# Performance work log

Measured on AMD Instinct MI355X. Metric: run time of the kernel, lower is better.

## Reference

```python
import jax, jax.numpy as jnp
import numpy as np

D_MODEL = 1024
NUM_HEADS = 16
D_K = D_MODEL // NUM_HEADS
THETA = 10000.0
B, T = 4, 2048


def apply_rope(x, positions):
    # x: [B, h, T, d_k], positions: [B, T] int
    half = D_K // 2
    inv_freq = 1.0 / (THETA ** (jnp.arange(half, dtype=jnp.float32) * 2.0 / D_K))  # [half]
    ang = positions.astype(jnp.float32)[:, None, :, None] * inv_freq  # [B,1,T,half]
    cos, sin = jnp.cos(ang), jnp.sin(ang)
    x1, x2 = x[..., 0::2], x[..., 1::2]  # even/odd interleaved pairs
    r1 = x1 * cos - x2 * sin
    r2 = x1 * sin + x2 * cos
    return jnp.stack([r1, r2], axis=-1).reshape(x.shape)


def setup_inputs() -> dict:
    key = jax.random.key(0)
    ks = jax.random.split(key, 5)
    scale = 1.0 / np.sqrt(D_MODEL)
    return {
        "in_features": jax.random.normal(ks[0], (B, T, D_MODEL), dtype=jnp.float32),
        "token_positions": jnp.broadcast_to(jnp.arange(T, dtype=jnp.int64), (B, T)),
        "Wq": jax.random.normal(ks[1], (D_MODEL, D_MODEL), dtype=jnp.float32) * scale,
        "Wk": jax.random.normal(ks[2], (D_MODEL, D_MODEL), dtype=jnp.float32) * scale,
        "Wv": jax.random.normal(ks[3], (D_MODEL, D_MODEL), dtype=jnp.float32) * scale,
        "Wo": jax.random.normal(ks[4], (D_MODEL, D_MODEL), dtype=jnp.float32) * scale,
    }


def reference(in_features, token_positions, Wq, Wk, Wv, Wo):
    x = in_features  # [B, T, d_model]
    # Linear stores weight [out, in]; y = x @ W.T (no bias)
    def proj(W):
        y = jnp.einsum('btd,ed->bte', x, W)
        return y.reshape(B, T, NUM_HEADS, D_K).transpose(0, 2, 1, 3)  # [B,h,T,d_k]
    Q, K, V = proj(Wq), proj(Wk), proj(Wv)
    Q = apply_rope(Q, token_positions)
    K = apply_rope(K, token_positions)
    scores = jnp.einsum('bhqd,bhkd->bhqk', Q, K) / jnp.sqrt(jnp.float32(D_K))
    causal = jnp.tril(jnp.ones((T, T), dtype=bool))  # True where allowed
    scores = jnp.where(causal, scores, jnp.float32(-1e30))
    attn = jax.nn.softmax(scores, axis=-1)
    heads = jnp.einsum('bhqk,bhkd->bhqd', attn, V)  # [B,h,T,d_k]
    out = heads.transpose(0, 2, 1, 3).reshape(B, T, D_MODEL)
    return jnp.einsum('btd,ed->bte', out, Wo)
```

## Files before the change

kernel.cpp:

```cpp
#include <hip/hip_runtime.h>
#include <cstdint>
#include <cstddef>

typedef unsigned short ushort_t;
typedef __attribute__((ext_vector_type(8))) short short8;
typedef __attribute__((ext_vector_type(4))) float f32x4;
typedef __attribute__((ext_vector_type(4))) _Float16 half4;
typedef __attribute__((ext_vector_type(8))) _Float16 half8;
typedef __attribute__((ext_vector_type(2))) _Float16 half2;
typedef __attribute__((ext_vector_type(2))) __fp16 fp16v2;
struct half4x2 { half4 lo, hi; };
struct half2x2 { half2 lo, hi; };

__device__ __forceinline__ unsigned short f2bf(float f) {
    unsigned u = __float_as_uint(f);
    u += 0x7fffu + ((u >> 16) & 1u);
    return (unsigned short)(u >> 16);
}
__device__ __forceinline__ float bf2f(unsigned short h) {
    return __uint_as_float((unsigned)h << 16);
}
__device__ __forceinline__ ushort_t f2h(float f) {
    _Float16 h = (_Float16)f;
    return __builtin_bit_cast(unsigned short, h);
}
__device__ __forceinline__ f32x4 zero4() {
    f32x4 z; z[0]=0.f; z[1]=0.f; z[2]=0.f; z[3]=0.f; return z;
}
__device__ __forceinline__ half4 pk4(float a, float b, float cc, float d) {
    half2x2 t;
    t.lo = __builtin_bit_cast(half2, (fp16v2)__builtin_amdgcn_cvt_pkrtz(a, b));
    t.hi = __builtin_bit_cast(half2, (fp16v2)__builtin_amdgcn_cvt_pkrtz(cc, d));
    return __builtin_bit_cast(half4, t);
}
__device__ __forceinline__ void gld_lds16(const ushort_t* g, ushort_t* l) {
    __builtin_amdgcn_global_load_lds(
        (const __attribute__((address_space(1))) void*)g,
        (__attribute__((address_space(3))) void*)l, 16, 0, 0);
}

__global__ void cvt_all(const float* __restrict__ x,
                        const float* __restrict__ wq, const float* __restrict__ wk,
                        const float* __restrict__ wv, const float* __restrict__ wo,
                        ushort_t* __restrict__ xb,
                        ushort_t* __restrict__ wqb, ushort_t* __restrict__ wkb,
                        ushort_t* __restrict__ wvb, ushort_t* __restrict__ wob,
                        float2* __restrict__ tab) {
    int idx = blockIdx.x * 256 + threadIdx.x;
    if (idx >= 3145728) {
        int i = idx - 3145728;
        int t = i >> 5, p = i & 31;
        float freq = __expf((float)p * -0.2878231366242557f);
        float sn, cs;
        sincosf((float)t * freq, &sn, &cs);
        tab[i] = make_float2(cs, sn);
        return;
    }
    const float* src; ushort_t* dst; int off;
    if (idx < 2097152) { src = x; dst = xb; off = idx; }
    else {
        int r = idx - 2097152;
        int w = r >> 18;
        off = r & 262143;
        src = (w == 0) ? wq : (w == 1) ? wk : (w == 2) ? wv : wo;
        dst = (w == 0) ? wqb : (w == 1) ? wkb : (w == 2) ? wvb : wob;
    }
    float4 v = ((const float4*)src)[off];
    ushort_t o[4];
    o[0] = f2bf(v.x); o[1] = f2bf(v.y); o[2] = f2bf(v.z); o[3] = f2bf(v.w);
    *(ushort4*)(dst + 4*(size_t)off) = *(const ushort4*)o;
}

__device__ __forceinline__ void gemm_core(const ushort_t* __restrict__ A,
                                          const ushort_t* __restrict__ W,
                                          ushort_t* As, ushort_t* Bs,
                                          int m0, int n0, f32x4 (&acc)[4][4]) {
    const int tid  = threadIdx.x;
    const int wave = tid >> 6, lane = tid & 63;
    const int wm = (wave >> 1) * 64, wn = (wave & 1) * 64;
    const int q = lane >> 4, c = lane & 15;
    const int srow = lane >> 3;
    const int gch  = (lane & 7) ^ srow;

    const ushort_t* ag = A + (size_t)(m0 + wave*8 + srow) * 1024 + gch*8;
    const ushort_t* bg = W + (size_t)(n0 + wave*8 + srow) * 1024 + gch*8;
    ushort_t* al = As + wave*512;
    ushort_t* bl = Bs + wave*512;

    for (int k0 = 0; k0 < 1024; k0 += 64) {
        __syncthreads();
#pragma unroll
        for (int n = 0; n < 4; ++n) gld_lds16(ag + (size_t)n*32768 + k0, al + n*2048);
#pragma unroll
        for (int n = 0; n < 4; ++n) gld_lds16(bg + (size_t)n*32768 + k0, bl + n*2048);
        asm volatile("s_waitcnt vmcnt(0)" ::: "memory");
        __syncthreads();

#pragma unroll
        for (int sk = 0; sk < 2; ++sk) {
            short8 af[4], bf[4];
#pragma unroll
            for (int i = 0; i < 4; ++i) {
                int row = wm + i*16 + c;
                af[i] = *(const short8*)(As + row*64 + (((sk*4 + q) ^ (row & 7)) * 8));
            }
#pragma unroll
            for (int j = 0; j < 4; ++j) {
                int row = wn + j*16 + c;
                bf[j] = *(const short8*)(Bs + row*64 + (((sk*4 + q) ^ (row & 7)) * 8));
            }
#pragma unroll
            for (int i = 0; i < 4; ++i)
#pragma unroll
                for (int j = 0; j < 4; ++j)
                    acc[i][j] = __builtin_amdgcn_mfma_f32_16x16x32_bf16(af[i], bf[j], acc[i][j], 0, 0, 0);
        }
    }
}

__device__ __forceinline__ void gemm_pipe256(const ushort_t* __restrict__ A,
                                             const ushort_t* __restrict__ W,
                                             ushort_t* __restrict__ As,
                                             ushort_t* __restrict__ Bs,
                                             int m0, int n0, f32x4 (&acc)[4][4]) {
    const int tid  = threadIdx.x;
    const int wave = tid >> 6, lane = tid & 63;
    const int wm = (wave >> 1) * 64, wn = (wave & 1) * 64;
    const int q = lane >> 4, c = lane & 15;
    const int srow = lane >> 3;
    const int gch  = (lane & 7) ^ srow;

    const ushort_t* ag = A + (size_t)(m0 + wave * 8 + srow) * 1024 + gch * 8;
    const ushort_t* bg = W + (size_t)(n0 + wave * 8 + srow) * 1024 + gch * 8;
    ushort_t* adst = As + wave * 512;
    ushort_t* bdst = Bs + wave * 512;

#pragma unroll
    for (int n = 0; n < 4; ++n) gld_lds16(ag + (size_t)n * 65536,      adst + n * 4096);
#pragma unroll
    for (int n = 0; n < 2; ++n) gld_lds16(bg + (size_t)n * 65536,      bdst + n * 4096);
#pragma unroll
    for (int n = 0; n < 4; ++n) gld_lds16(ag + (size_t)n * 65536 + 64, adst + 16384 + n * 4096);
#pragma unroll
    for (int n = 0; n < 2; ++n) gld_lds16(bg + (size_t)n * 65536 + 64, bdst + 8192 + n * 4096);
    asm volatile("s_waitcnt vmcnt(6)" ::: "memory");
    __builtin_amdgcn_s_barrier();

    const int ch0 = (q ^ (c & 7)) * 8;
    const int ch1 = ((4 + q) ^ (c & 7)) * 8;
    int cur = 0;
    for (int t = 0; t < 16; ++t) {
        const int nx2 = (cur >= 1) ? cur - 1 : 2;
        const ushort_t* ab = As + cur * 16384 + (wm + c) * 64;
        const ushort_t* bb = Bs + cur * 8192  + (wn + c) * 64;
        const int kc = (t + 2) * 64;
        const bool pf = (t < 14);
        short8 af[4], bf[4];

#pragma unroll
        for (int i = 0; i < 4; ++i) af[i] = *(const short8*)(ab + i * 1024 + ch0);
#pragma unroll
        for (int j = 0; j < 4; ++j) bf[j] = *(const short8*)(bb + j * 1024 + ch0);
        if (pf) {
            gld_lds16(ag + kc,           adst + nx2 * 16384);
            gld_lds16(ag + 65536 + kc,   adst + nx2 * 16384 + 4096);
            gld_lds16(bg + kc,           bdst + nx2 * 8192);
        }
        __builtin_amdgcn_s_barrier();
        asm volatile("s_waitcnt lgkmcnt(0)" ::: "memory");
        __builtin_amdgcn_s_setprio(1);
#pragma unroll
        for (int i = 0; i < 4; ++i)
#pragma unroll
            for (int j = 0; j < 4; ++j)
                acc[i][j] = __builtin_amdgcn_mfma_f32_16x16x32_bf16(af[i], bf[j], acc[i][j], 0, 0, 0);
        __builtin_amdgcn_s_setprio(0);
        __builtin_amdgcn_s_barrier();

#pragma unroll
        for (int i = 0; i < 4; ++i) af[i] = *(const short8*)(ab + i * 1024 + ch1);
#pragma unroll
        for (int j = 0; j < 4; ++j) bf[j] = *(const short8*)(bb + j * 1024 + ch1);
        if (pf) {
            gld_lds16(ag + 131072 + kc,  adst + nx2 * 16384 + 8192);
            gld_lds16(ag + 196608 + kc,  adst + nx2 * 16384 + 12288);
            gld_lds16(bg + 65536 + kc,   bdst + nx2 * 8192 + 4096);
        }
        __builtin_amdgcn_s_barrier();
        asm volatile("s_waitcnt lgkmcnt(0)" ::: "memory");
        __builtin_amdgcn_s_setprio(1);
#pragma unroll
        for (int i = 0; i < 4; ++i)
#pragma unroll
            for (int j = 0; j < 4; ++j)
                acc[i][j] = __builtin_amdgcn_mfma_f32_16x16x32_bf16(af[i], bf[j], acc[i][j], 0, 0, 0);
        __builtin_amdgcn_s_setprio(0);
        if (pf) { asm volatile("s_waitcnt vmcnt(6)" ::: "memory"); }
        else    { asm volatile("s_waitcnt vmcnt(0)" ::: "memory"); }
        __builtin_amdgcn_s_barrier();
        cur = (cur == 2) ? 0 : cur + 1;
    }
}

__global__ __launch_bounds__(256) void gemm_qkv_kernel(
    const ushort_t* __restrict__ X, const ushort_t* __restrict__ Wq,
    const ushort_t* __restrict__ Wk, const ushort_t* __restrict__ Wv,
    const float2* __restrict__ tab,
    ushort_t* __restrict__ Q, ushort_t* __restrict__ Kt, ushort_t* __restrict__ Vt) {
    __shared__ ushort_t As[128*64];
    __shared__ ushort_t Bs[128*64];
    const int orig = blockIdx.x;
    const int wg = (orig & 7) * 192 + (orig >> 3);
    const int my = wg / 24;
    const int n24 = wg - my * 24;
    const int which = n24 >> 3;
    const ushort_t* W = (which == 0) ? Wq : (which == 1) ? Wk : Wv;
    const int m0 = my * 128;
    const int nloc0 = (n24 & 7) * 128;

    f32x4 acc[4][4];
#pragma unroll
    for (int i = 0; i < 4; ++i)
#pragma unroll
        for (int j = 0; j < 4; ++j) acc[i][j] = zero4();

    gemm_core(X, W, As, Bs, m0, nloc0, acc);

    const int lane = threadIdx.x & 63, wave = threadIdx.x >> 6;
    const int q = lane >> 4, c = lane & 15;
    const int wm = (wave >> 1) * 64, wn = (wave & 1) * 64;
    const float scale = (which == 0) ? 0.18033688011112042f : 1.0f;

#pragma unroll
    for (int i = 0; i < 4; ++i)
#pragma unroll
        for (int j = 0; j < 4; ++j) {
            int nn = nloc0 + wn + j*16 + c;
            int d = nn & 63, h = nn >> 6;
            int pidx = d >> 1;
            float sgn = (d & 1) ? 1.f : -1.f;
#pragma unroll
            for (int r = 0; r < 4; ++r) {
                int mm = m0 + wm + i*16 + q*4 + r;
                int b = mm >> 11, t = mm & 2047;
                float val = acc[i][j][r];
                if (which == 0) {
                    float partner = __shfl_xor(val, 1);
                    float2 cs = tab[t * 32 + pidx];
                    val = (val * cs.x + sgn * partner * cs.y) * scale;
                    Q[((size_t)((b << 4) + h) * 2048 + t) * 64 + d] = f2bf(val);
                } else if (which == 1) {
                    float partner = __shfl_xor(val, 1);
                    float2 cs = tab[t * 32 + pidx];
                    val = val * cs.x + sgn * partner * cs.y;
                    int kb = t >> 6, jn = (t >> 4) & 3, cc2 = t & 15;
                    int ks2 = d >> 5, qq2 = (d >> 3) & 3, e = d & 7;
                    int lane2 = qq2 * 16 + cc2;
                    Kt[((((size_t)((b << 4) + h) * 32 + kb) * 8 + jn * 2 + ks2) << 9) + lane2 * 8 + e] = f2bf(val);
                } else {
                    int kb = t >> 6, kl = t & 63;
                    int jn = kl >> 4, qq2 = (kl >> 2) & 3;
                    int e = ((jn & 1) << 2) | (kl & 3);
                    int p = ((d >> 4) << 1) | (jn >> 1);
                    int lane2 = qq2 * 16 + (d & 15);
                    Vt[((((size_t)((b << 4) + h) * 32 + kb) * 8 + p) << 9) + lane2 * 8 + e] = f2h(val);
                }
            }
        }
}

__global__ __launch_bounds__(512) void gemm_out_kernel(
    const ushort_t* __restrict__ A, const ushort_t* __restrict__ Wo,
    float* __restrict__ OUT) {
    __shared__ ushort_t As[3 * 16384];
    __shared__ ushort_t Bs[3 * 8192];
    const int orig = blockIdx.x;
    const int wg = (orig & 7) * 32 + (orig >> 3);
    const int m0 = (wg >> 3) * 256, n0 = (wg & 7) * 128;

    f32x4 acc[4][4];
#pragma unroll
    for (int i = 0; i < 4; ++i)
#pragma unroll
        for (int j = 0; j < 4; ++j) acc[i][j] = zero4();

    gemm_pipe256(A, Wo, As, Bs, m0, n0, acc);

    const int lane = threadIdx.x & 63, wave = threadIdx.x >> 6;
    const int q = lane >> 4, c = lane & 15;
    const int wm = (wave >> 1) * 64, wn = (wave & 1) * 64;
#pragma unroll
    for (int i = 0; i < 4; ++i)
#pragma unroll
        for (int j = 0; j < 4; ++j)
#pragma unroll
            for (int r = 0; r < 4; ++r) {
                int mm = m0 + wm + i*16 + q*4 + r;
                int nn = n0 + wn + j*16 + c;
                OUT[(size_t)mm * 1024 + nn] = acc[i][j][r];
            }
}

__global__ __launch_bounds__(256, 3) void flash_kernel(
    const ushort_t* __restrict__ Q, const ushort_t* __restrict__ Kt,
    const ushort_t* __restrict__ Vt, ushort_t* __restrict__ AO) {
    __shared__ ushort_t Ks[2][4096];
    __shared__ ushort_t Vs[2][4096];
    const int bh = blockIdx.x;
    const int c0 = 15 - blockIdx.y;
    const int w  = threadIdx.x >> 6, lane = threadIdx.x & 63;
    const int q = lane >> 4, c = lane & 15;
    const int qlo = c0 * 128;
    const int nt  = 2 * c0 + 2;
    const int wq0 = qlo + w * 32;
    const int b = bh >> 4, hh = bh & 15;

    const ushort_t* Qp = Q + (size_t)bh * 131072;
    const ushort_t* kt0 = Kt + (size_t)bh * 131072;
    const ushort_t* vt0 = Vt + (size_t)bh * 131072;

    short8 qf[2][2];
#pragma unroll
    for (int m = 0; m < 2; ++m)
#pragma unroll
        for (int ks = 0; ks < 2; ++ks)
            qf[m][ks] = *(const short8*)(Qp + (size_t)(wq0 + m*16 + c) * 64 + ks * 32 + q * 8);

    f32x4 ot[2][4];
#pragma unroll
    for (int m = 0; m < 2; ++m)
#pragma unroll
        for (int dj = 0; dj < 4; ++dj) ot[m][dj] = zero4();
    float lpart[2] = {0.f, 0.f};

#pragma unroll
    for (int s = 0; s < 2; ++s) {
        gld_lds16(kt0 + (s*4 + w)*512 + lane*8, &Ks[0][(s*4 + w)*512]);
        gld_lds16(vt0 + (s*4 + w)*512 + lane*8, &Vs[0][(s*4 + w)*512]);
    }
    asm volatile("s_waitcnt vmcnt(0)" ::: "memory");
    __syncthreads();

    for (int kb = 0; kb < nt; ++kb) {
        const int cur = kb & 1;
        if (kb + 1 < nt) {
            const ushort_t* kt = kt0 + (size_t)(kb + 1) * 4096;
            const ushort_t* vt = vt0 + (size_t)(kb + 1) * 4096;
#pragma unroll
            for (int s = 0; s < 2; ++s) {
                gld_lds16(kt + (s*4 + w)*512 + lane*8, &Ks[cur ^ 1][(s*4 + w)*512]);
                gld_lds16(vt + (s*4 + w)*512 + lane*8, &Vs[cur ^ 1][(s*4 + w)*512]);
            }
        }

        if (kb * 64 <= wq0 + 31) {
            const ushort_t* Kb = &Ks[cur][0];
            const ushort_t* Vb = &Vs[cur][0];
            f32x4 st[2][4];
#pragma unroll
            for (int jn = 0; jn < 4; ++jn) {
                short8 kf0 = *(const short8*)(Kb + (jn*2+0)*512 + lane*8);
                short8 kf1 = *(const short8*)(Kb + (jn*2+1)*512 + lane*8);
#pragma unroll
                for (int m = 0; m < 2; ++m) {
                    f32x4 t0 = __builtin_amdgcn_mfma_f32_16x16x32_bf16(kf0, qf[m][0], zero4(), 0, 0, 0);
                    st[m][jn] = __builtin_amdgcn_mfma_f32_16x16x32_bf16(kf1, qf[m][1], t0, 0, 0, 0);
                }
            }
            if (kb * 64 + 63 > wq0) {
#pragma unroll
                for (int m = 0; m < 2; ++m) {
                    int query = wq0 + m * 16 + c;
#pragma unroll
                    for (int jn = 0; jn < 4; ++jn)
#pragma unroll
                        for (int r = 0; r < 4; ++r)
                            if (kb * 64 + jn * 16 + q * 4 + r > query) st[m][jn][r] = -1e30f;
                }
            }
            half4 pa[2][4];
#pragma unroll
            for (int m = 0; m < 2; ++m)
#pragma unroll
                for (int jn = 0; jn < 4; ++jn) {
                    float p0 = exp2f(st[m][jn][0]), p1 = exp2f(st[m][jn][1]);
                    float p2 = exp2f(st[m][jn][2]), p3 = exp2f(st[m][jn][3]);
                    lpart[m] += (p0 + p1) + (p2 + p3);
                    pa[m][jn] = pk4(p0, p1, p2, p3);
                }
#pragma unroll
            for (int jnp = 0; jnp < 2; ++jnp)
#pragma unroll
                for (int dj = 0; dj < 4; ++dj) {
                    half8 vv8 = __builtin_bit_cast(half8,
                        *(const short8*)(Vb + (dj*2 + jnp)*512 + lane*8));
#pragma unroll
                    for (int m = 0; m < 2; ++m) {
                        half4x2 pb;
                        pb.lo = pa[m][2*jnp];
                        pb.hi = pa[m][2*jnp+1];
                        ot[m][dj] = __builtin_amdgcn_mfma_f32_16x16x32_f16(
                            vv8, __builtin_bit_cast(half8, pb), ot[m][dj], 0, 0, 0);
                    }
                }
        }

        asm volatile("s_waitcnt vmcnt(0)" ::: "memory");
        __syncthreads();
    }

#pragma unroll
    for (int m = 0; m < 2; ++m) {
        float l = lpart[m];
        l += __shfl_xor(l, 16);
        l += __shfl_xor(l, 32);
        float inv = 1.f / l;
        int t = wq0 + m * 16 + c;
        ushort_t* base = AO + ((size_t)b * 2048 + t) * 1024 + hh * 64;
#pragma unroll
        for (int dj = 0; dj < 4; ++dj) {
            ushort4 o;
            o.x = f2bf(ot[m][dj][0] * inv);
            o.y = f2bf(ot[m][dj][1] * inv);
            o.z = f2bf(ot[m][dj][2] * inv);
            o.w = f2bf(ot[m][dj][3] * inv);
            *(ushort4*)(base + dj * 16 + q * 4) = o;
        }
    }
}

extern "C" void kernel_launch(void* const* d_in, const int* in_sizes, int n_in,
                              void* d_out, int out_size, void* d_ws, size_t ws_size,
                              hipStream_t stream) {
    const float* x  = (const float*)d_in[0];
    const float* Wq = (const float*)d_in[2];
    const float* Wk = (const float*)d_in[3];
    const float* Wv = (const float*)d_in[4];
    const float* Wo = (const float*)d_in[5];
    float* out = (float*)d_out;

    ushort_t* ws  = (ushort_t*)d_ws;
    ushort_t* Xb  = ws;
    ushort_t* Qb  = ws + 8388608;
    ushort_t* Ktb = ws + 16777216;
    ushort_t* Vtb = ws + 25165824;
    ushort_t* Wqb = ws + 33554432;
    ushort_t* Wkb = Wqb + 1048576;
    ushort_t* Wvb = Wkb + 1048576;
    ushort_t* Wob = Wvb + 1048576;
    float2*   tab = (float2*)(ws + 37748736);

    cvt_all<<<12544, 256, 0, stream>>>(x, Wq, Wk, Wv, Wo, Xb, Wqb, Wkb, Wvb, Wob, tab);

    gemm_qkv_kernel<<<1536, 256, 0, stream>>>(Xb, Wqb, Wkb, Wvb, tab, Qb, Ktb, Vtb);

    flash_kernel<<<dim3(64, 16), 256, 0, stream>>>(Qb, Ktb, Vtb, Xb);

    gemm_out_kernel<<<256, 512, 0, stream>>>(Xb, Wob, out);
}
```

Measured before the change: 284.3 us.

## Double-buffer LDS tiles in QKV projection GEMM to overlap loads with MFMA

Replaces the single-buffered K-loop of the QKV projection GEMM with a two-stage ping-pong. The next 64-wide K slice is issued into the alternate LDS buffer before the MFMAs run on the current one. This is meant to hide global-to-LDS load latency and drop one barrier per iteration. It doubles the LDS footprint per block, which may lower occupancy. Completion of the async loads now depends on the barrier's implicit wait, since the explicit vmcnt(0) wait was removed.

```diff
diff --git a/kernel.cpp b/kernel.cpp
--- a/kernel.cpp
+++ b/kernel.cpp
@@ -71,10 +71,10 @@
     *(ushort4*)(dst + 4*(size_t)off) = *(const ushort4*)o;
 }
 
-__device__ __forceinline__ void gemm_core(const ushort_t* __restrict__ A,
-                                          const ushort_t* __restrict__ W,
-                                          ushort_t* As, ushort_t* Bs,
-                                          int m0, int n0, f32x4 (&acc)[4][4]) {
+__device__ __forceinline__ void gemm_core_db(const ushort_t* __restrict__ A,
+                                             const ushort_t* __restrict__ W,
+                                             ushort_t* As, ushort_t* Bs,
+                                             int m0, int n0, f32x4 (&acc)[4][4]) {
     const int tid  = threadIdx.x;
     const int wave = tid >> 6, lane = tid & 63;
     const int wm = (wave >> 1) * 64, wn = (wave & 1) * 64;
@@ -87,27 +87,37 @@
     ushort_t* al = As + wave*512;
     ushort_t* bl = Bs + wave*512;
 
+#pragma unroll
+    for (int n = 0; n < 4; ++n) gld_lds16(ag + (size_t)n*32768, al + n*2048);
+#pragma unroll
+    for (int n = 0; n < 4; ++n) gld_lds16(bg + (size_t)n*32768, bl + n*2048);
+    __syncthreads();
+
+    int cur = 0;
     for (int k0 = 0; k0 < 1024; k0 += 64) {
-        __syncthreads();
-#pragma unroll
-        for (int n = 0; n < 4; ++n) gld_lds16(ag + (size_t)n*32768 + k0, al + n*2048);
-#pragma unroll
-        for (int n = 0; n < 4; ++n) gld_lds16(bg + (size_t)n*32768 + k0, bl + n*2048);
-        asm volatile("s_waitcnt vmcnt(0)" ::: "memory");
-        __syncthreads();
-
+        if (k0 + 64 < 1024) {
+            const int nb = cur ^ 1;
+#pragma unroll
+            for (int n = 0; n < 4; ++n)
+                gld_lds16(ag + (size_t)n*32768 + k0 + 64, al + nb*8192 + n*2048);
+#pragma unroll
+            for (int n = 0; n < 4; ++n)
+                gld_lds16(bg + (size_t)n*32768 + k0 + 64, bl + nb*8192 + n*2048);
+        }
+        const ushort_t* Ab = As + cur*8192;
+        const ushort_t* Bb = Bs + cur*8192;
 #pragma unroll
         for (int sk = 0; sk < 2; ++sk) {
             short8 af[4], bf[4];
 #pragma unroll
             for (int i = 0; i < 4; ++i) {
                 int row = wm + i*16 + c;
-                af[i] = *(const short8*)(As + row*64 + (((sk*4 + q) ^ (row & 7)) * 8));
+                af[i] = *(const short8*)(Ab + row*64 + (((sk*4 + q) ^ (row & 7)) * 8));
             }
 #pragma unroll
             for (int j = 0; j < 4; ++j) {
                 int row = wn + j*16 + c;
-                bf[j] = *(const short8*)(Bs + row*64 + (((sk*4 + q) ^ (row & 7)) * 8));
+                bf[j] = *(const short8*)(Bb + row*64 + (((sk*4 + q) ^ (row & 7)) * 8));
             }
 #pragma unroll
             for (int i = 0; i < 4; ++i)
@@ -115,6 +125,8 @@
                 for (int j = 0; j < 4; ++j)
                     acc[i][j] = __builtin_amdgcn_mfma_f32_16x16x32_bf16(af[i], bf[j], acc[i][j], 0, 0, 0);
         }
+        __syncthreads();
+        cur ^= 1;
     }
 }
 
@@ -207,8 +219,8 @@
     const ushort_t* __restrict__ Wk, const ushort_t* __restrict__ Wv,
     const float2* __restrict__ tab,
     ushort_t* __restrict__ Q, ushort_t* __restrict__ Kt, ushort_t* __restrict__ Vt) {
-    __shared__ ushort_t As[128*64];
-    __shared__ ushort_t Bs[128*64];
+    __shared__ ushort_t As[2 * 8192];
+    __shared__ ushort_t Bs[2 * 8192];
     const int orig = blockIdx.x;
     const int wg = (orig & 7) * 192 + (orig >> 3);
     const int my = wg / 24;
@@ -224,7 +236,7 @@
 #pragma unroll
         for (int j = 0; j < 4; ++j) acc[i][j] = zero4();
 
-    gemm_core(X, W, As, Bs, m0, nloc0, acc);
+    gemm_core_db(X, W, As, Bs, m0, nloc0, acc);
 
     const int lane = threadIdx.x & 63, wave = threadIdx.x >> 6;
     const int q = lane >> 4, c = lane & 15;
```

Measured after the change: 278.5 us. 2.1% less time.

## Double-buffer QKV GEMM shared-memory tiles with a K=32 prefetch pipeline

Applied to the files above, without the earlier changes.

The QKV projection GEMM core is rewritten so that the next K=32 slice of A and W is loaded into a second LDS buffer while MFMAs run on the current one. The previous version loaded a K=64 tile with a full vmcnt(0) wait and two barriers per step. The new version splits the same LDS footprint into two halves with a new XOR swizzle for 32-wide rows. The aim is to hide global-to-LDS latency behind matrix math. The cost is twice as many loop iterations and barriers, and it relies on the barrier to wait for the async LDS loads to finish.

```diff
diff --git a/kernel.cpp b/kernel.cpp
--- a/kernel.cpp
+++ b/kernel.cpp
@@ -71,50 +71,57 @@
     *(ushort4*)(dst + 4*(size_t)off) = *(const ushort4*)o;
 }
 
-__device__ __forceinline__ void gemm_core(const ushort_t* __restrict__ A,
-                                          const ushort_t* __restrict__ W,
-                                          ushort_t* As, ushort_t* Bs,
-                                          int m0, int n0, f32x4 (&acc)[4][4]) {
+__device__ __forceinline__ void gemm_core_db32(const ushort_t* __restrict__ A,
+                                               const ushort_t* __restrict__ W,
+                                               ushort_t* As, ushort_t* Bs,
+                                               int m0, int n0, f32x4 (&acc)[4][4]) {
     const int tid  = threadIdx.x;
     const int wave = tid >> 6, lane = tid & 63;
     const int wm = (wave >> 1) * 64, wn = (wave & 1) * 64;
     const int q = lane >> 4, c = lane & 15;
-    const int srow = lane >> 3;
-    const int gch  = (lane & 7) ^ srow;
-
-    const ushort_t* ag = A + (size_t)(m0 + wave*8 + srow) * 1024 + gch*8;
-    const ushort_t* bg = W + (size_t)(n0 + wave*8 + srow) * 1024 + gch*8;
-    ushort_t* al = As + wave*512;
-    ushort_t* bl = Bs + wave*512;
-
-    for (int k0 = 0; k0 < 1024; k0 += 64) {
+    const int srow = lane >> 2;
+    const int gch  = (lane & 3) ^ ((lane >> 3) & 3);
+
+    const ushort_t* ag0 = A + (size_t)(m0 +      wave*16 + srow) * 1024 + gch*8;
+    const ushort_t* ag1 = A + (size_t)(m0 + 64 + wave*16 + srow) * 1024 + gch*8;
+    const ushort_t* bg0 = W + (size_t)(n0 +      wave*16 + srow) * 1024 + gch*8;
+    const ushort_t* bg1 = W + (size_t)(n0 + 64 + wave*16 + srow) * 1024 + gch*8;
+    ushort_t* a0 = As + wave*512;
+    ushort_t* a1 = As + 2048 + wave*512;
+    ushort_t* b0 = Bs + wave*512;
+    ushort_t* b1 = Bs + 2048 + wave*512;
+
+    gld_lds16(ag0, a0); gld_lds16(ag1, a1);
+    gld_lds16(bg0, b0); gld_lds16(bg1, b1);
+    __syncthreads();
+
+    const int ch = (q ^ ((c >> 1) & 3)) * 8;
+    int cur = 0;
+    for (int t = 0; t < 32; ++t) {
+        if (t + 1 < 32) {
+            const int nb = cur ^ 1;
+            const int kc = (t + 1) * 32;
+            gld_lds16(ag0 + kc, a0 + nb*4096);
+            gld_lds16(ag1 + kc, a1 + nb*4096);
+            gld_lds16(bg0 + kc, b0 + nb*4096);
+            gld_lds16(bg1 + kc, b1 + nb*4096);
+        }
+        const ushort_t* Ab = As + cur*4096;
+        const ushort_t* Bb = Bs + cur*4096;
+        short8 af[4], bf[4];
+#pragma unroll
+        for (int i = 0; i < 4; ++i)
+            af[i] = *(const short8*)(Ab + (wm + i*16 + c)*32 + ch);
+#pragma unroll
+        for (int j = 0; j < 4; ++j)
+            bf[j] = *(const short8*)(Bb + (wn + j*16 + c)*32 + ch);
+#pragma unroll
+        for (int i = 0; i < 4; ++i)
+#pragma unroll
+            for (int j = 0; j < 4; ++j)
+                acc[i][j] = __builtin_amdgcn_mfma_f32_16x16x32_bf16(af[i], bf[j], acc[i][j], 0, 0, 0);
         __syncthreads();
-#pragma unroll
-        for (int n = 0; n < 4; ++n) gld_lds16(ag + (size_t)n*32768 + k0, al + n*2048);
-#pragma unroll
-        for (int n = 0; n < 4; ++n) gld_lds16(bg + (size_t)n*32768 + k0, bl + n*2048);
-        asm volatile("s_waitcnt vmcnt(0)" ::: "memory");
-        __syncthreads();
-
-#pragma unroll
-        for (int sk = 0; sk < 2; ++sk) {
-            short8 af[4], bf[4];
-#pragma unroll
-            for (int i = 0; i < 4; ++i) {
-                int row = wm + i*16 + c;
-                af[i] = *(const short8*)(As + row*64 + (((sk*4 + q) ^ (row & 7)) * 8));
-            }
-#pragma unroll
-            for (int j = 0; j < 4; ++j) {
-                int row = wn + j*16 + c;
-                bf[j] = *(const short8*)(Bs + row*64 + (((sk*4 + q) ^ (row & 7)) * 8));
-            }
-#pragma unroll
-            for (int i = 0; i < 4; ++i)
-#pragma unroll
-                for (int j = 0; j < 4; ++j)
-                    acc[i][j] = __builtin_amdgcn_mfma_f32_16x16x32_bf16(af[i], bf[j], acc[i][j], 0, 0, 0);
-        }
+        cur ^= 1;
     }
 }
 
@@ -207,8 +214,8 @@
     const ushort_t* __restrict__ Wk, const ushort_t* __restrict__ Wv,
     const float2* __restrict__ tab,
     ushort_t* __restrict__ Q, ushort_t* __restrict__ Kt, ushort_t* __restrict__ Vt) {
-    __shared__ ushort_t As[128*64];
-    __shared__ ushort_t Bs[128*64];
+    __shared__ ushort_t As[2 * 4096];
+    __shared__ ushort_t Bs[2 * 4096];
     const int orig = blockIdx.x;
     const int wg = (orig & 7) * 192 + (orig >> 3);
     const int my = wg / 24;
@@ -224,7 +231,7 @@
 #pragma unroll
         for (int j = 0; j < 4; ++j) acc[i][j] = zero4();
 
-    gemm_core(X, W, As, Bs, m0, nloc0, acc);
+    gemm_core_db32(X, W, As, Bs, m0, nloc0, acc);
 
     const int lane = threadIdx.x & 63, wave = threadIdx.x >> 6;
     const int q = lane >> 4, c = lane & 15;
```

Result: faster. 271.9 us (-4.4%).
